# Optimization experiments

Measured on AMD Instinct MI355X. Metric: run time of the kernel, lower is better.

The kernel has to match this reference:

```python
import jax, jax.numpy as jnp
import numpy as np

UNIT_LEN = 16   # tokens per unit
DEPTH = 8       # units per path (path depth)
H = 256; NH = 8; DH = H // NH; FF = 1024; NL = 2; V = 32000; PAD = 0


def _pe(L, d):
    # standard sinusoidal positional encoding, seq-first [L,1,d]
    pos = jnp.arange(L, dtype=jnp.float32)[:, None]
    div = jnp.exp(jnp.arange(0, d, 2, dtype=jnp.float32) * (-np.log(10000.0) / d))
    pe = jnp.zeros((L, d), jnp.float32)
    pe = pe.at[:, 0::2].set(jnp.sin(pos * div)).at[:, 1::2].set(jnp.cos(pos * div))
    return pe[:, None, :]


def _ln(x, s, b):
    m = x.mean(-1, keepdims=True)
    v = jnp.mean((x - m) ** 2, -1, keepdims=True)
    return (x - m) * jax.lax.rsqrt(v + 1e-5) * s + b


def _layer(x, kpm, qkv_w, qkv_b, out_w, out_b, ln1_s, ln1_b, ff1_w, ff1_b, ff2_w, ff2_b, ln2_s, ln2_b):
    # x: [L,B,H] (seq-first, like torch TransformerEncoderLayer); kpm: [B,L] True = pad
    L, B, _ = x.shape
    qkv = x @ qkv_w.T + qkv_b
    q, k, v = jnp.split(qkv, 3, axis=-1)
    q = q.reshape(L, B, NH, DH); k = k.reshape(L, B, NH, DH); v = v.reshape(L, B, NH, DH)
    s = jnp.einsum('qbhd,kbhd->bhqk', q, k) / np.sqrt(DH)
    s = jnp.where(kpm[:, None, None, :], -1e9, s)
    a = jax.nn.softmax(s, axis=-1)
    o = jnp.einsum('bhqk,kbhd->qbhd', a, v).reshape(L, B, H) @ out_w.T + out_b
    x = _ln(x + o, ln1_s, ln1_b)
    f = jax.nn.relu(x @ ff1_w.T + ff1_b) @ ff2_w.T + ff2_b
    return _ln(x + f, ln2_s, ln2_b)


def _encoder(x, kpm, p):
    for i in range(p[0].shape[0]):
        x = _layer(x, kpm, *(w[i] for w in p))
    return x


def _mk_enc(key):
    ks = jax.random.split(key, 4)
    sc = 0.02
    return (jax.random.normal(ks[0], (NL, 3 * H, H)) * sc, jnp.zeros((NL, 3 * H)),
            jax.random.normal(ks[1], (NL, H, H)) * sc, jnp.zeros((NL, H)),
            jnp.ones((NL, H)), jnp.zeros((NL, H)),
            jax.random.normal(ks[2], (NL, FF, H)) * sc, jnp.zeros((NL, FF)),
            jax.random.normal(ks[3], (NL, H, FF)) * sc, jnp.zeros((NL, H)),
            jnp.ones((NL, H)), jnp.zeros((NL, H)))


NAMES = ['qkv_w', 'qkv_b', 'out_w', 'out_b', 'ln1_s', 'ln1_b', 'ff1_w', 'ff1_b', 'ff2_w', 'ff2_b', 'ln2_s', 'ln2_b']


def setup_inputs():
    key = jax.random.key(0)
    k = jax.random.split(key, 6)
    B = 8; UPD = 32; PPD = 64
    units = jax.random.randint(k[0], (UNIT_LEN, B * UPD), 0, V)
    paths = jax.random.randint(k[1], (DEPTH, B * PPD), 0, UPD)
    emb = jax.random.normal(k[2], (V, H)) * 0.02
    d = {'units': units, 'paths': paths, 'unit_per_data': UPD, 'path_per_data': PPD, 'emb': emb}
    for n_, a in zip(NAMES, _mk_enc(k[3])):
        d['ep_' + n_] = a
    for n_, a in zip(NAMES, _mk_enc(k[4])):
        d['od_' + n_] = a
    return d


def _forward(units, paths, unit_per_data, path_per_data, emb, ep, od):
    # _unit_to_path: expand each path into its units' token sequences (vectorized gather).
    P = paths.shape[1]
    col = (jnp.arange(P) // path_per_data) * unit_per_data + paths       # [DEPTH, P] global unit column
    ctx = units[:, col]                                                  # [UNIT_LEN, DEPTH, P]
    ctx = jnp.transpose(ctx, (1, 0, 2)).reshape(DEPTH * UNIT_LEN, P)     # concat units along the path
    mask = ctx == PAD                                                    # expaths key-padding mask
    x = emb[ctx] + _pe(ctx.shape[0], H)
    expaths = _encoder(x, mask.T, ep)
    # _cut_batch: concat each sample's unit token sequences into one order sequence.
    nb = units.shape[1] // unit_per_data
    order_tok = units.reshape(UNIT_LEN, nb, unit_per_data).transpose(2, 0, 1).reshape(unit_per_data * UNIT_LEN, nb)
    omask = order_tok == PAD
    y = emb[order_tok] + _pe(order_tok.shape[0], H)
    order_enc = _encoder(y, omask.T, od)
    return expaths, order_enc


def reference(units, paths, unit_per_data, path_per_data, emb,
              ep_qkv_w, ep_qkv_b, ep_out_w, ep_out_b, ep_ln1_s, ep_ln1_b, ep_ff1_w, ep_ff1_b, ep_ff2_w, ep_ff2_b, ep_ln2_s, ep_ln2_b,
              od_qkv_w, od_qkv_b, od_out_w, od_out_b, od_ln1_s, od_ln1_b, od_ff1_w, od_ff1_b, od_ff2_w, od_ff2_b, od_ln2_s, od_ln2_b):
    ep = (ep_qkv_w, ep_qkv_b, ep_out_w, ep_out_b, ep_ln1_s, ep_ln1_b, ep_ff1_w, ep_ff1_b, ep_ff2_w, ep_ff2_b, ep_ln2_s, ep_ln2_b)
    od = (od_qkv_w, od_qkv_b, od_out_w, od_out_b, od_ln1_s, od_ln1_b, od_ff1_w, od_ff1_b, od_ff2_w, od_ff2_b, od_ln2_s, od_ln2_b)
    return _forward(units, paths, unit_per_data, path_per_data, emb, ep, od)
```

## Files before the change

### kernel.cpp

```cpp
#include <hip/hip_runtime.h>
#include <math.h>

#define H      256
#define NH     8
#define DH     32
#define FFDIM  1024
#define L1     128
#define B1     512
#define L2     512
#define B2     8
#define N1     (L1*B1)
#define N2     (L2*B2)
#define RT1    (N1/128)
#define RT2    (N2/128)
#define QSCL   0.25506602273492887f

typedef unsigned short u16;
typedef unsigned short ushort4_t __attribute__((ext_vector_type(4)));
typedef unsigned short ushort8_t __attribute__((ext_vector_type(8)));
typedef short          short8_t  __attribute__((ext_vector_type(8)));
typedef float          f32x4     __attribute__((ext_vector_type(4)));

__device__ __forceinline__ float bf2f(u16 u) {
    union { unsigned int i; float f; } v; v.i = ((unsigned int)u) << 16; return v.f;
}
__device__ __forceinline__ u16 f2bf(float f) {
    union { float f; unsigned int i; } v; v.f = f;
    unsigned int x = v.i;
    return (u16)((x + 0x7fffu + ((x >> 16) & 1u)) >> 16);
}
__device__ __forceinline__ unsigned cvt_pk_bf16(float lo, float hi) {
    unsigned r;
    asm("v_cvt_pk_bf16_f32 %0, %1, %2" : "=v"(r) : "v"(lo), "v"(hi));
    return r;
}

__global__ __launch_bounds__(256) void k_f2bf8(
    const float* __restrict__ s0, const float* __restrict__ s1,
    const float* __restrict__ s2, const float* __restrict__ s3,
    const float* __restrict__ s4, const float* __restrict__ s5,
    const float* __restrict__ s6, const float* __restrict__ s7,
    u16* __restrict__ out)
{
    const int cums[9] = {0, 393216, 524288, 1048576, 1572864,
                         1966080, 2097152, 2621440, 3145728};
    const float* srcs[8] = {s0, s1, s2, s3, s4, s5, s6, s7};
    const int gbase = blockIdx.x * 1024;
    int seg = 0;
    #pragma unroll
    for (int i = 1; i < 8; ++i) if (gbase >= cums[i]) seg = i;
    const int idx = gbase + threadIdx.x * 4;
    const int off = idx - cums[seg];
    const float fs = ((seg == 0 || seg == 4) && (off % 196608) < 65536)
                   ? QSCL : 1.0f;
    const float4 v = *(const float4*)(srcs[seg] + off);
    ushort4_t o;
    o.x = f2bf(v.x * fs); o.y = f2bf(v.y * fs);
    o.z = f2bf(v.z * fs); o.w = f2bf(v.w * fs);
    *(ushort4_t*)(out + idx) = o;
}

__global__ __launch_bounds__(256) void k_scaleb(
    const float* __restrict__ b1, const float* __restrict__ b2,
    float* __restrict__ out)
{
    const int i = blockIdx.x * 256 + threadIdx.x;
    const float* src = (i < 1536) ? b1 : b2;
    const int j = (i < 1536) ? i : i - 1536;
    float v = src[j];
    if ((j % 768) < 256) v *= QSCL;
    out[i] = v;
}

__global__ __launch_bounds__(256) void k_gather(
    const int* __restrict__ units, const int* __restrict__ paths,
    const float* __restrict__ emb,
    u16* __restrict__ x1, u16* __restrict__ x2,
    int* __restrict__ tokb1, int* __restrict__ tokb2)
{
    const int wave = threadIdx.x >> 6, lane = threadIdx.x & 63;
    const int t = blockIdx.x * 4 + wave;
    int tokid, l;
    u16* xp; int* tokp;
    if (t < N1) {
        l = t / B1; const int b = t - l * B1;
        const int d = l >> 4, u = l & 15;
        const int col = (b >> 6) * 32 + paths[d * 512 + b];
        tokid = units[u * 256 + col];
        xp = x1 + (size_t)t * H; tokp = tokb1 + t;
    } else {
        const int t2 = t - N1;
        l = t2 / B2; const int b = t2 - l * B2;
        const int w = l >> 4, u = l & 15;
        tokid = units[u * 256 + b * 32 + w];
        xp = x2 + (size_t)t2 * H; tokp = tokb2 + t2;
    }
    if (lane == 0) *tokp = tokid;
    const int c = lane * 4;
    const float4 e = *(const float4*)(emb + (size_t)tokid * H + c);
    const float i0 = (float)(c >> 1);
    const float a0 = (float)l * expf(-0.07195578415606394f * i0);
    const float a1 = (float)l * expf(-0.07195578415606394f * (i0 + 1.0f));
    ushort4_t o;
    o.x = f2bf(e.x + sinf(a0));
    o.y = f2bf(e.y + cosf(a0));
    o.z = f2bf(e.z + sinf(a1));
    o.w = f2bf(e.w + cosf(a1));
    *(ushort4_t*)(xp + c) = o;
}

#define BUF_U16 8192
__global__ __launch_bounds__(256) void k_gemm_mfma(
    const u16* __restrict__ X1, const u16* __restrict__ X2,
    const u16* __restrict__ W1, const u16* __restrict__ W2,
    const float* __restrict__ b1, const float* __restrict__ b2,
    u16* __restrict__ Y1, u16* __restrict__ Y2,
    int K, int M, int relu)
{
    __shared__ __align__(16) u16 smem[17408];
    const int t = threadIdx.x;
    const int mtiles = M >> 7;
    const int nwg = gridDim.x;
    const int bid = blockIdx.x;
    const int wg = (bid & 7) * (nwg >> 3) + (bid >> 3);
    const int rt = wg / mtiles;
    const int bn = (wg % mtiles) * 128;
    const u16* X; const u16* W; const float* bias; u16* Y; int bm;
    if (rt < RT1) { X = X1; W = W1; bias = b1; Y = Y1; bm = rt * 128; }
    else          { X = X2; W = W2; bias = b2; Y = Y2; bm = (rt - RT1) * 128; }
    const int wave = t >> 6, lane = t & 63;
    const int wr = (wave >> 1) * 64, wc = (wave & 1) * 64;
    const int lrow = lane & 15;
    const int lg   = lane >> 4;

    const u16* gx[2]; const u16* gw[2];
    int ldsxo[2], ldswo[2];
    #pragma unroll
    for (int i = 0; i < 2; ++i) {
        const int c = wave * 2 + i;
        const int r = c * 16 + (lane >> 2);
        const int s = (lane & 3) ^ ((r >> 1) & 3);
        gx[i] = X + (size_t)(bm + r) * K + s * 8;
        gw[i] = W + (size_t)(bn + r) * K + s * 8;
        ldsxo[i] = c * 512;
        ldswo[i] = 4096 + c * 512;
    }
    int aoff[4], boff[4];
    #pragma unroll
    for (int m = 0; m < 4; ++m) {
        const int R = wr + m * 16 + lrow;
        aoff[m] = R * 32 + ((lg ^ ((R >> 1) & 3)) * 8);
    }
    #pragma unroll
    for (int n = 0; n < 4; ++n) {
        const int R = wc + n * 16 + lrow;
        boff[n] = 4096 + R * 32 + ((lg ^ ((R >> 1) & 3)) * 8);
    }

    f32x4 acc[4][4] = {};
    const int nt = K >> 5;

    #pragma unroll
    for (int i = 0; i < 2; ++i) {
        __builtin_amdgcn_global_load_lds(gx[i], &smem[ldsxo[i]], 16, 0, 0);
        __builtin_amdgcn_global_load_lds(gw[i], &smem[ldswo[i]], 16, 0, 0);
        gx[i] += 32; gw[i] += 32;
    }
    __syncthreads();

    int cur = 0;
    for (int ts = 0; ts < nt; ++ts) {
        if (ts + 1 < nt) {
            const int nb = (cur ^ 1) * BUF_U16;
            #pragma unroll
            for (int i = 0; i < 2; ++i) {
                __builtin_amdgcn_global_load_lds(gx[i], &smem[nb + ldsxo[i]], 16, 0, 0);
                __builtin_amdgcn_global_load_lds(gw[i], &smem[nb + ldswo[i]], 16, 0, 0);
                gx[i] += 32; gw[i] += 32;
            }
        }
        const int cb = cur * BUF_U16;
        short8_t a[4], b[4];
        #pragma unroll
        for (int m = 0; m < 4; ++m) a[m] = *(const short8_t*)&smem[cb + aoff[m]];
        #pragma unroll
        for (int n = 0; n < 4; ++n) b[n] = *(const short8_t*)&smem[cb + boff[n]];
        #pragma unroll
        for (int m = 0; m < 4; ++m)
            #pragma unroll
            for (int n = 0; n < 4; ++n)
                acc[m][n] = __builtin_amdgcn_mfma_f32_16x16x32_bf16(
                    a[m], b[n], acc[m][n], 0, 0, 0);
        __syncthreads();
        cur ^= 1;
    }

    float bv[4];
    #pragma unroll
    for (int n = 0; n < 4; ++n) bv[n] = bias[bn + wc + n * 16 + lrow];
    const int r0 = (lane >> 4) * 4;

    #pragma unroll
    for (int n = 0; n < 4; ++n) {
        const int lc = wc + n * 16 + lrow;
        #pragma unroll
        for (int m = 0; m < 4; ++m) {
            const int lr = wr + m * 16 + r0;
            #pragma unroll
            for (int j = 0; j < 4; ++j) {
                float v = acc[m][n][j] + bv[n];
                if (relu) v = fmaxf(v, 0.f);
                smem[(lr + j) * 136 + lc] = f2bf(v);
            }
        }
    }
    __syncthreads();
    #pragma unroll
    for (int it = 0; it < 8; ++it) {
        const int slot = it * 256 + t;
        const int row = slot >> 4;
        const int seg = (slot & 15) * 8;
        *(ushort8_t*)(Y + (size_t)(bm + row) * M + bn + seg) =
            *(const ushort8_t*)&smem[row * 136 + seg];
    }
}

__global__ __launch_bounds__(256) void k_attn_mfma(
    const u16* __restrict__ qkv1, const u16* __restrict__ qkv2,
    const int* __restrict__ tok1, const int* __restrict__ tok2,
    u16* __restrict__ out1, u16* __restrict__ out2)
{
    __shared__ __align__(16) u16 Ks[128][40];
    __shared__ __align__(16) u16 Vt[32][136];
    __shared__ __align__(16) u16 Pl[128][40];
    __shared__ int msk[128];
    const int t = threadIdx.x;
    const int wave = t >> 6, lane = t & 63;
    const int lq = lane & 15, lg = lane >> 4;
    const int bid = blockIdx.x;
    const u16* qkv; const int* tok; u16* out;
    int L, Bv, b, h, qt;
    if (bid < B1 * NH) {
        qkv = qkv1; tok = tok1; out = out1; L = L1; Bv = B1;
        qt = 0; b = bid >> 3; h = bid & 7;
    } else {
        const int r = bid - B1 * NH;
        qkv = qkv2; tok = tok2; out = out2; L = L2; Bv = B2;
        qt = r >> 6; const int bh = r & 63; b = bh >> 3; h = bh & 7;
    }
    const int q0 = qt * 128 + wave * 32;

    short8_t qf[2];
    #pragma unroll
    for (int n = 0; n < 2; ++n)
        qf[n] = *(const short8_t*)(qkv +
            (size_t)((q0 + n * 16 + lq) * Bv + b) * 768 + h * DH + lg * 8);

    f32x4 o[2][2] = {};
    float mrun[2] = {-1e9f, -1e9f};
    float lrun[2] = {0.f, 0.f};

    for (int kt = 0; kt < L; kt += 128) {
        #pragma unroll
        for (int it = 0; it < 2; ++it) {
            const int slot = t + it * 256;
            const int row = slot >> 2;
            const int seg = (slot & 3) * 8;
            const u16* base = qkv + (size_t)((kt + row) * Bv + b) * 768 + 256 + h * DH + seg;
            *(ushort8_t*)&Ks[row][seg] = *(const ushort8_t*)base;
            const ushort8_t v8 = *(const ushort8_t*)(base + 256);
            #pragma unroll
            for (int e = 0; e < 8; ++e) Vt[seg + e][row] = v8[e];
        }
        if (t < 128) msk[t] = tok[(size_t)(kt + t) * Bv + b];
        __syncthreads();

        uint2 preg[2][8];
        #pragma unroll
        for (int n = 0; n < 2; ++n) {
            f32x4 s[8];
            #pragma unroll
            for (int mp = 0; mp < 8; ++mp) {
                const short8_t kf = *(const short8_t*)&Ks[mp * 16 + lq][lg * 8];
                s[mp] = __builtin_amdgcn_mfma_f32_16x16x32_bf16(
                    kf, qf[n], (f32x4){0.f, 0.f, 0.f, 0.f}, 0, 0, 0);
            }
            float mx = -3.0e38f;
            #pragma unroll
            for (int mp = 0; mp < 8; ++mp) {
                #pragma unroll
                for (int j = 0; j < 4; ++j) {
                    float v = s[mp][j];
                    v = (msk[mp * 16 + lg * 4 + j] == 0) ? -1e9f : v;
                    s[mp][j] = v;
                    mx = fmaxf(mx, v);
                }
            }
            mx = fmaxf(mx, __shfl_xor(mx, 16));
            mx = fmaxf(mx, __shfl_xor(mx, 32));
            const float mnew = fmaxf(mrun[n], mx);
            const float fac = exp2f(mrun[n] - mnew);
            mrun[n] = mnew;
            lrun[n] *= fac;
            #pragma unroll
            for (int dt = 0; dt < 2; ++dt)
                #pragma unroll
                for (int j = 0; j < 4; ++j) o[dt][n][j] *= fac;
            float lsum = 0.f;
            #pragma unroll
            for (int mp = 0; mp < 8; ++mp) {
                const float p0 = exp2f(s[mp][0] - mnew);
                const float p1 = exp2f(s[mp][1] - mnew);
                const float p2 = exp2f(s[mp][2] - mnew);
                const float p3 = exp2f(s[mp][3] - mnew);
                lsum += (p0 + p1) + (p2 + p3);
                preg[n][mp].x = cvt_pk_bf16(p0, p1);
                preg[n][mp].y = cvt_pk_bf16(p2, p3);
            }
            lsum += __shfl_xor(lsum, 16);
            lsum += __shfl_xor(lsum, 32);
            lrun[n] += lsum;
        }

        #pragma unroll
        for (int kk = 0; kk < 4; ++kk) {
            #pragma unroll
            for (int n = 0; n < 2; ++n) {
                u16* prow = &Pl[wave * 32 + n * 16 + lq][0];
                *(uint2*)(prow + lg * 4)      = preg[n][2 * kk];
                *(uint2*)(prow + 16 + lg * 4) = preg[n][2 * kk + 1];
            }
            short8_t pf[2];
            #pragma unroll
            for (int n = 0; n < 2; ++n)
                pf[n] = *(const short8_t*)&Pl[wave * 32 + n * 16 + lq][lg * 8];
            #pragma unroll
            for (int dt = 0; dt < 2; ++dt) {
                const short8_t vf = *(const short8_t*)&Vt[dt * 16 + lq][kk * 32 + lg * 8];
                #pragma unroll
                for (int n = 0; n < 2; ++n)
                    o[dt][n] = __builtin_amdgcn_mfma_f32_16x16x32_bf16(
                        vf, pf[n], o[dt][n], 0, 0, 0);
            }
        }
        __syncthreads();
    }

    #pragma unroll
    for (int n = 0; n < 2; ++n) {
        const float inv = 1.f / lrun[n];
        const int q = q0 + n * 16 + lq;
        u16* op = out + (size_t)(q * Bv + b) * H + h * DH;
        #pragma unroll
        for (int dt = 0; dt < 2; ++dt)
            #pragma unroll
            for (int jj = 0; jj < 2; ++jj) {
                const unsigned pk = cvt_pk_bf16(o[dt][n][jj*2] * inv,
                                                o[dt][n][jj*2+1] * inv);
                *(unsigned*)(op + dt * 16 + lg * 4 + jj * 2) = pk;
            }
    }
}

__global__ __launch_bounds__(256) void k_add_ln(
    const u16* __restrict__ x1, const u16* __restrict__ x2,
    const u16* __restrict__ r1, const u16* __restrict__ r2,
    const float* __restrict__ gs1, const float* __restrict__ gs2,
    const float* __restrict__ gb1, const float* __restrict__ gb2,
    u16* __restrict__ y1, u16* __restrict__ y2)
{
    const int wave = threadIdx.x >> 6, lane = threadIdx.x & 63;
    size_t row = (size_t)blockIdx.x * 4 + wave;
    const u16 *x, *r; const float *gs, *gb; u16* y;
    if (row < N1) { x = x1; r = r1; gs = gs1; gb = gb1; y = y1; }
    else { row -= N1; x = x2; r = r2; gs = gs2; gb = gb2; y = y2; }
    const int c = lane * 4;
    const ushort4_t xv = *(const ushort4_t*)(x + row * H + c);
    const ushort4_t rv = *(const ushort4_t*)(r + row * H + c);
    float v[4] = { bf2f(xv.x) + bf2f(rv.x), bf2f(xv.y) + bf2f(rv.y),
                   bf2f(xv.z) + bf2f(rv.z), bf2f(xv.w) + bf2f(rv.w) };
    float sum = v[0] + v[1] + v[2] + v[3];
    float sq  = v[0]*v[0] + v[1]*v[1] + v[2]*v[2] + v[3]*v[3];
    #pragma unroll
    for (int off = 1; off < 64; off <<= 1) {
        sum += __shfl_xor(sum, off);
        sq  += __shfl_xor(sq, off);
    }
    const float mean = sum * (1.f / H);
    const float var  = sq * (1.f / H) - mean * mean;
    const float is   = rsqrtf(var + 1e-5f);
    const float4 sv = *(const float4*)(gs + c);
    const float4 bv = *(const float4*)(gb + c);
    ushort4_t o;
    o.x = f2bf((v[0] - mean) * is * sv.x + bv.x);
    o.y = f2bf((v[1] - mean) * is * sv.y + bv.y);
    o.z = f2bf((v[2] - mean) * is * sv.z + bv.z);
    o.w = f2bf((v[3] - mean) * is * sv.w + bv.w);
    *(ushort4_t*)(y + row * H + c) = o;
}

__global__ __launch_bounds__(256) void k_add_ln_f32(
    const u16* __restrict__ x1, const u16* __restrict__ x2,
    const u16* __restrict__ r1, const u16* __restrict__ r2,
    const float* __restrict__ gs1, const float* __restrict__ gs2,
    const float* __restrict__ gb1, const float* __restrict__ gb2,
    float* __restrict__ y)
{
    const int wave = threadIdx.x >> 6, lane = threadIdx.x & 63;
    const size_t grow = (size_t)blockIdx.x * 4 + wave;
    const int c = lane * 4;
    float* yp = y + grow * H + c;
    size_t row = grow;
    const u16 *x, *r; const float *gs, *gb;
    if (row < N1) { x = x1; r = r1; gs = gs1; gb = gb1; }
    else { row -= N1; x = x2; r = r2; gs = gs2; gb = gb2; }
    const ushort4_t xv = *(const ushort4_t*)(x + row * H + c);
    const ushort4_t rv = *(const ushort4_t*)(r + row * H + c);
    float v[4] = { bf2f(xv.x) + bf2f(rv.x), bf2f(xv.y) + bf2f(rv.y),
                   bf2f(xv.z) + bf2f(rv.z), bf2f(xv.w) + bf2f(rv.w) };
    float sum = v[0] + v[1] + v[2] + v[3];
    float sq  = v[0]*v[0] + v[1]*v[1] + v[2]*v[2] + v[3]*v[3];
    #pragma unroll
    for (int off = 1; off < 64; off <<= 1) {
        sum += __shfl_xor(sum, off);
        sq  += __shfl_xor(sq, off);
    }
    const float mean = sum * (1.f / H);
    const float var  = sq * (1.f / H) - mean * mean;
    const float is   = rsqrtf(var + 1e-5f);
    const float4 sv = *(const float4*)(gs + c);
    const float4 bv = *(const float4*)(gb + c);
    float4 o;
    o.x = (v[0] - mean) * is * sv.x + bv.x;
    o.y = (v[1] - mean) * is * sv.y + bv.y;
    o.z = (v[2] - mean) * is * sv.z + bv.z;
    o.w = (v[3] - mean) * is * sv.w + bv.w;
    *(float4*)yp = o;
}

extern "C" void kernel_launch(void* const* d_in, const int* in_sizes, int n_in,
                              void* d_out, int out_size, void* d_ws, size_t ws_size,
                              hipStream_t stream)
{
    const int* units = (const int*)d_in[0];
    const int* paths = (const int*)d_in[1];
    const float* emb = (const float*)d_in[4];
    const float* const* ep = (const float* const*)(d_in + 5);
    const float* const* od = (const float* const*)(d_in + 17);
    float* out = (float*)d_out;

    u16* bufX1   = (u16*)d_ws;
    u16* bufX2   = bufX1 + (size_t)N1 * H;
    u16* bufBig1 = bufX2 + (size_t)N2 * H;
    u16* bufBig2 = bufBig1 + (size_t)N1 * FFDIM;
    u16* bufO1   = bufBig2 + (size_t)N2 * FFDIM;
    u16* bufO2   = bufO1 + (size_t)N1 * H;
    int* tokb1   = (int*)(bufO2 + (size_t)N2 * H);
    int* tokb2   = tokb1 + N1;
    u16* wbuf    = (u16*)(tokb2 + N2);
    const int wqkv = 2 * 768 * H, wout = 2 * H * H,
              wff1 = 2 * FFDIM * H, wff2 = 2 * H * FFDIM;
    const int encstride = wqkv + wout + wff1 + wff2;
    float* qbias = (float*)(wbuf + 2 * (size_t)encstride);

    k_f2bf8<<<(2 * encstride) / 1024, 256, 0, stream>>>(
        ep[0], ep[2], ep[6], ep[8], od[0], od[2], od[6], od[8], wbuf);
    k_scaleb<<<12, 256, 0, stream>>>(ep[1], od[1], qbias);

    k_gather<<<(N1 + N2) / 4, 256, 0, stream>>>(units, paths, emb,
                                                bufX1, bufX2, tokb1, tokb2);

    for (int layer = 0; layer < 2; ++layer) {
        const u16* wb1 = wbuf;
        const u16* wb2 = wbuf + (size_t)encstride;
        const u16* qkvw1 = wb1 + (size_t)layer * 768 * H;
        const u16* qkvw2 = wb2 + (size_t)layer * 768 * H;
        const u16* outw1 = wb1 + wqkv + (size_t)layer * H * H;
        const u16* outw2 = wb2 + wqkv + (size_t)layer * H * H;
        const u16* ff1w1 = wb1 + wqkv + wout + (size_t)layer * FFDIM * H;
        const u16* ff1w2 = wb2 + wqkv + wout + (size_t)layer * FFDIM * H;
        const u16* ff2w1 = wb1 + wqkv + wout + wff1 + (size_t)layer * H * FFDIM;
        const u16* ff2w2 = wb2 + wqkv + wout + wff1 + (size_t)layer * H * FFDIM;
        const float* qkvb1 = qbias + (size_t)layer * 768;
        const float* qkvb2 = qbias + 1536 + (size_t)layer * 768;
        const float* outb1 = ep[3] + (size_t)layer * H;
        const float* outb2 = od[3] + (size_t)layer * H;
        const float* ln1s1 = ep[4] + (size_t)layer * H;
        const float* ln1s2 = od[4] + (size_t)layer * H;
        const float* ln1b1 = ep[5] + (size_t)layer * H;
        const float* ln1b2 = od[5] + (size_t)layer * H;
        const float* ff1b1 = ep[7] + (size_t)layer * FFDIM;
        const float* ff1b2 = od[7] + (size_t)layer * FFDIM;
        const float* ff2b1 = ep[9] + (size_t)layer * H;
        const float* ff2b2 = od[9] + (size_t)layer * H;
        const float* ln2s1 = ep[10] + (size_t)layer * H;
        const float* ln2s2 = od[10] + (size_t)layer * H;
        const float* ln2b1 = ep[11] + (size_t)layer * H;
        const float* ln2b2 = od[11] + (size_t)layer * H;

        k_gemm_mfma<<<(RT1 + RT2) * (768 / 128), 256, 0, stream>>>(
            bufX1, bufX2, qkvw1, qkvw2, qkvb1, qkvb2, bufBig1, bufBig2, H, 768, 0);
        k_attn_mfma<<<B1 * NH + B2 * NH * (L2 / 128), 256, 0, stream>>>(
            bufBig1, bufBig2, tokb1, tokb2, bufO1, bufO2);
        k_gemm_mfma<<<(RT1 + RT2) * (H / 128), 256, 0, stream>>>(
            bufO1, bufO2, outw1, outw2, outb1, outb2, bufBig1, bufBig2, H, H, 0);
        k_add_ln<<<(N1 + N2) / 4, 256, 0, stream>>>(
            bufX1, bufX2, bufBig1, bufBig2, ln1s1, ln1s2, ln1b1, ln1b2, bufX1, bufX2);
        k_gemm_mfma<<<(RT1 + RT2) * (FFDIM / 128), 256, 0, stream>>>(
            bufX1, bufX2, ff1w1, ff1w2, ff1b1, ff1b2, bufBig1, bufBig2, H, FFDIM, 1);
        k_gemm_mfma<<<(RT1 + RT2) * (H / 128), 256, 0, stream>>>(
            bufBig1, bufBig2, ff2w1, ff2w2, ff2b1, ff2b2, bufO1, bufO2, FFDIM, H, 0);
        if (layer == 1)
            k_add_ln_f32<<<(N1 + N2) / 4, 256, 0, stream>>>(
                bufX1, bufX2, bufO1, bufO2, ln2s1, ln2s2, ln2b1, ln2b2, out);
        else
            k_add_ln<<<(N1 + N2) / 4, 256, 0, stream>>>(
                bufX1, bufX2, bufO1, bufO2, ln2s1, ln2s2, ln2b1, ln2b2, bufX1, bufX2);
    }
}
```

Measured before the change: 565.6 us.

## Fuse output-projection and FF2 GEMMs with residual add and LayerNorm

Adds a GEMM kernel with 64x256 output tiles that covers the full hidden width, so each block can add the bias and residual, compute row mean and variance across two waves through shared memory, and write the LayerNorm result directly. It replaces the separate GEMM plus add-LN kernels, removing one intermediate write and read of the activation tensor and one launch per LN. The fused kernel uses larger tiles, so fewer blocks and more registers, and it reads the residual from the same buffer it overwrites. That in-place write is safe only because each block reads its own rows before writing them.

```diff
diff --git a/kernel.cpp b/kernel.cpp
--- a/kernel.cpp
+++ b/kernel.cpp
@@ -225,6 +225,213 @@
     }
 }
 
+#define BUF2_U16 10240
+template<int FP32OUT>
+__global__ __launch_bounds__(256) void k_gemm_ln(
+    const u16* __restrict__ X1, const u16* __restrict__ X2,
+    const u16* __restrict__ W1, const u16* __restrict__ W2,
+    const float* __restrict__ b1, const float* __restrict__ b2,
+    const u16* __restrict__ R1, const u16* __restrict__ R2,
+    const float* __restrict__ gs1, const float* __restrict__ gs2,
+    const float* __restrict__ gb1, const float* __restrict__ gb2,
+    u16* __restrict__ Y1, u16* __restrict__ Y2, float* __restrict__ Yf,
+    int K)
+{
+    __shared__ __align__(16) u16 smem[2 * BUF2_U16];
+    const int t = threadIdx.x;
+    const int nwg = gridDim.x;
+    const int bid = blockIdx.x;
+    const int wg = (bid & 7) * (nwg >> 3) + (bid >> 3);
+    const u16* X; const u16* W; const float* bias; const u16* res;
+    const float* gs; const float* gb; u16* Y; int bm; size_t growbase;
+    if (wg < N1 / 64) {
+        X = X1; W = W1; bias = b1; res = R1; gs = gs1; gb = gb1; Y = Y1;
+        bm = wg * 64; growbase = (size_t)bm;
+    } else {
+        X = X2; W = W2; bias = b2; res = R2; gs = gs2; gb = gb2; Y = Y2;
+        bm = (wg - N1 / 64) * 64; growbase = (size_t)N1 + bm;
+    }
+    const int wave = t >> 6, lane = t & 63;
+    const int wrow = (wave >> 1) * 32;
+    const int wcol = (wave & 1) * 128;
+    const int lrow = lane & 15;
+    const int lg   = lane >> 4;
+
+    const u16* gsrc[5]; int ldso[5];
+    #pragma unroll
+    for (int i = 0; i < 5; ++i) {
+        const int c = wave * 5 + i;
+        const int rr = lane >> 2;
+        const int s  = lane & 3;
+        if (c < 4) {
+            const int r = c * 16 + rr;
+            gsrc[i] = X + (size_t)(bm + r) * K + ((s ^ ((r >> 1) & 3)) * 8);
+        } else {
+            const int r = (c - 4) * 16 + rr;
+            gsrc[i] = W + (size_t)r * K + ((s ^ ((r >> 1) & 3)) * 8);
+        }
+        ldso[i] = c * 512;
+    }
+    int aoff[2], boff[8];
+    #pragma unroll
+    for (int m = 0; m < 2; ++m) {
+        const int R = wrow + m * 16 + lrow;
+        aoff[m] = R * 32 + ((lg ^ ((R >> 1) & 3)) * 8);
+    }
+    #pragma unroll
+    for (int n = 0; n < 8; ++n) {
+        const int R = wcol + n * 16 + lrow;
+        boff[n] = 2048 + R * 32 + ((lg ^ ((R >> 1) & 3)) * 8);
+    }
+
+    f32x4 acc[2][8] = {};
+    const int nt = K >> 5;
+
+    #pragma unroll
+    for (int i = 0; i < 5; ++i) {
+        __builtin_amdgcn_global_load_lds(gsrc[i], &smem[ldso[i]], 16, 0, 0);
+        gsrc[i] += 32;
+    }
+    __syncthreads();
+
+    int cur = 0;
+    for (int ts = 0; ts < nt; ++ts) {
+        if (ts + 1 < nt) {
+            const int nb = (cur ^ 1) * BUF2_U16;
+            #pragma unroll
+            for (int i = 0; i < 5; ++i) {
+                __builtin_amdgcn_global_load_lds(gsrc[i], &smem[nb + ldso[i]], 16, 0, 0);
+                gsrc[i] += 32;
+            }
+        }
+        const int cb = cur * BUF2_U16;
+        short8_t a[2], b[8];
+        #pragma unroll
+        for (int m = 0; m < 2; ++m) a[m] = *(const short8_t*)&smem[cb + aoff[m]];
+        #pragma unroll
+        for (int n = 0; n < 8; ++n) b[n] = *(const short8_t*)&smem[cb + boff[n]];
+        #pragma unroll
+        for (int m = 0; m < 2; ++m)
+            #pragma unroll
+            for (int n = 0; n < 8; ++n)
+                acc[m][n] = __builtin_amdgcn_mfma_f32_16x16x32_bf16(
+                    a[m], b[n], acc[m][n], 0, 0, 0);
+        __syncthreads();
+        cur ^= 1;
+    }
+
+    float bv[8], gsv[8], gbv[8];
+    #pragma unroll
+    for (int n = 0; n < 8; ++n) {
+        const int col = wcol + n * 16 + lrow;
+        bv[n] = bias[col]; gsv[n] = gs[col]; gbv[n] = gb[col];
+    }
+
+    #pragma unroll
+    for (int it = 0; it < 8; ++it) {
+        const int slot = it * 256 + t;
+        const int row = slot >> 5;
+        const int seg = (slot & 31) * 8;
+        *(ushort8_t*)&smem[row * 264 + seg] =
+            *(const ushort8_t*)(res + (size_t)(bm + row) * 256 + seg);
+    }
+    __syncthreads();
+
+    float* sums = (float*)&smem[16896];
+
+    const int r0 = lg * 4;
+    #pragma unroll
+    for (int m = 0; m < 2; ++m) {
+        #pragma unroll
+        for (int j = 0; j < 4; ++j) {
+            const int rowl = wrow + m * 16 + r0 + j;
+            float s = 0.f, q = 0.f;
+            #pragma unroll
+            for (int n = 0; n < 8; ++n) {
+                const int col = wcol + n * 16 + lrow;
+                float v = acc[m][n][j] + bv[n] + bf2f(smem[rowl * 264 + col]);
+                acc[m][n][j] = v;
+                s += v; q += v * v;
+            }
+            #pragma unroll
+            for (int off = 1; off < 16; off <<= 1) {
+                s += __shfl_xor(s, off);
+                q += __shfl_xor(q, off);
+            }
+            if (lrow == 0) {
+                sums[rowl * 4 + (wave & 1) * 2 + 0] = s;
+                sums[rowl * 4 + (wave & 1) * 2 + 1] = q;
+            }
+        }
+    }
+    __syncthreads();
+
+    if (FP32OUT == 0) {
+        #pragma unroll
+        for (int m = 0; m < 2; ++m) {
+            #pragma unroll
+            for (int j = 0; j < 4; ++j) {
+                const int rowl = wrow + m * 16 + r0 + j;
+                const float s = sums[rowl * 4 + 0] + sums[rowl * 4 + 2];
+                const float q = sums[rowl * 4 + 1] + sums[rowl * 4 + 3];
+                const float mean = s * (1.f / 256.f);
+                const float var  = q * (1.f / 256.f) - mean * mean;
+                const float is   = rsqrtf(var + 1e-5f);
+                #pragma unroll
+                for (int n = 0; n < 8; ++n) {
+                    const int col = wcol + n * 16 + lrow;
+                    const float y = (acc[m][n][j] - mean) * is * gsv[n] + gbv[n];
+                    smem[rowl * 264 + col] = f2bf(y);
+                }
+            }
+        }
+        __syncthreads();
+        #pragma unroll
+        for (int it = 0; it < 8; ++it) {
+            const int slot = it * 256 + t;
+            const int row = slot >> 5;
+            const int seg = (slot & 31) * 8;
+            *(ushort8_t*)(Y + (size_t)(bm + row) * 256 + seg) =
+                *(const ushort8_t*)&smem[row * 264 + seg];
+        }
+    } else {
+        float* fstage = (float*)smem;
+        #pragma unroll
+        for (int h = 0; h < 2; ++h) {
+            if ((wave & 1) == h) {
+                #pragma unroll
+                for (int m = 0; m < 2; ++m) {
+                    #pragma unroll
+                    for (int j = 0; j < 4; ++j) {
+                        const int rowl = wrow + m * 16 + r0 + j;
+                        const float s = sums[rowl * 4 + 0] + sums[rowl * 4 + 2];
+                        const float q = sums[rowl * 4 + 1] + sums[rowl * 4 + 3];
+                        const float mean = s * (1.f / 256.f);
+                        const float var  = q * (1.f / 256.f) - mean * mean;
+                        const float is   = rsqrtf(var + 1e-5f);
+                        #pragma unroll
+                        for (int n = 0; n < 8; ++n) {
+                            const int col = n * 16 + lrow;
+                            const float y = (acc[m][n][j] - mean) * is * gsv[n] + gbv[n];
+                            fstage[rowl * 130 + col] = y;
+                        }
+                    }
+                }
+            }
+            __syncthreads();
+            #pragma unroll
+            for (int it = 0; it < 8; ++it) {
+                const int slot = it * 256 + t;
+                const int row = slot >> 5;
+                const int seg = (slot & 31) * 4;
+                *(float4*)(Yf + (growbase + row) * 256 + h * 128 + seg) =
+                    *(const float4*)&fstage[row * 130 + seg];
+            }
+            __syncthreads();
+        }
+    }
+}
+
 __global__ __launch_bounds__(256) void k_attn_mfma(
     const u16* __restrict__ qkv1, const u16* __restrict__ qkv2,
     const int* __restrict__ tok1, const int* __restrict__ tok2,
@@ -360,82 +567,6 @@
                 *(unsigned*)(op + dt * 16 + lg * 4 + jj * 2) = pk;
             }
     }
-}
-
-__global__ __launch_bounds__(256) void k_add_ln(
-    const u16* __restrict__ x1, const u16* __restrict__ x2,
-    const u16* __restrict__ r1, const u16* __restrict__ r2,
-    const float* __restrict__ gs1, const float* __restrict__ gs2,
-    const float* __restrict__ gb1, const float* __restrict__ gb2,
-    u16* __restrict__ y1, u16* __restrict__ y2)
-{
-    const int wave = threadIdx.x >> 6, lane = threadIdx.x & 63;
-    size_t row = (size_t)blockIdx.x * 4 + wave;
-    const u16 *x, *r; const float *gs, *gb; u16* y;
-    if (row < N1) { x = x1; r = r1; gs = gs1; gb = gb1; y = y1; }
-    else { row -= N1; x = x2; r = r2; gs = gs2; gb = gb2; y = y2; }
-    const int c = lane * 4;
-    const ushort4_t xv = *(const ushort4_t*)(x + row * H + c);
-    const ushort4_t rv = *(const ushort4_t*)(r + row * H + c);
-    float v[4] = { bf2f(xv.x) + bf2f(rv.x), bf2f(xv.y) + bf2f(rv.y),
-                   bf2f(xv.z) + bf2f(rv.z), bf2f(xv.w) + bf2f(rv.w) };
-    float sum = v[0] + v[1] + v[2] + v[3];
-    float sq  = v[0]*v[0] + v[1]*v[1] + v[2]*v[2] + v[3]*v[3];
-    #pragma unroll
-    for (int off = 1; off < 64; off <<= 1) {
-        sum += __shfl_xor(sum, off);
-        sq  += __shfl_xor(sq, off);
-    }
-    const float mean = sum * (1.f / H);
-    const float var  = sq * (1.f / H) - mean * mean;
-    const float is   = rsqrtf(var + 1e-5f);
-    const float4 sv = *(const float4*)(gs + c);
-    const float4 bv = *(const float4*)(gb + c);
-    ushort4_t o;
-    o.x = f2bf((v[0] - mean) * is * sv.x + bv.x);
-    o.y = f2bf((v[1] - mean) * is * sv.y + bv.y);
-    o.z = f2bf((v[2] - mean) * is * sv.z + bv.z);
-    o.w = f2bf((v[3] - mean) * is * sv.w + bv.w);
-    *(ushort4_t*)(y + row * H + c) = o;
-}
-
-__global__ __launch_bounds__(256) void k_add_ln_f32(
-    const u16* __restrict__ x1, const u16* __restrict__ x2,
-    const u16* __restrict__ r1, const u16* __restrict__ r2,
-    const float* __restrict__ gs1, const float* __restrict__ gs2,
-    const float* __restrict__ gb1, const float* __restrict__ gb2,
-    float* __restrict__ y)
-{
-    const int wave = threadIdx.x >> 6, lane = threadIdx.x & 63;
-    const size_t grow = (size_t)blockIdx.x * 4 + wave;
-    const int c = lane * 4;
-    float* yp = y + grow * H + c;
-    size_t row = grow;
-    const u16 *x, *r; const float *gs, *gb;
-    if (row < N1) { x = x1; r = r1; gs = gs1; gb = gb1; }
-    else { row -= N1; x = x2; r = r2; gs = gs2; gb = gb2; }
-    const ushort4_t xv = *(const ushort4_t*)(x + row * H + c);
-    const ushort4_t rv = *(const ushort4_t*)(r + row * H + c);
-    float v[4] = { bf2f(xv.x) + bf2f(rv.x), bf2f(xv.y) + bf2f(rv.y),
-                   bf2f(xv.z) + bf2f(rv.z), bf2f(xv.w) + bf2f(rv.w) };
-    float sum = v[0] + v[1] + v[2] + v[3];
-    float sq  = v[0]*v[0] + v[1]*v[1] + v[2]*v[2] + v[3]*v[3];
-    #pragma unroll
-    for (int off = 1; off < 64; off <<= 1) {
-        sum += __shfl_xor(sum, off);
-        sq  += __shfl_xor(sq, off);
-    }
-    const float mean = sum * (1.f / H);
-    const float var  = sq * (1.f / H) - mean * mean;
-    const float is   = rsqrtf(var + 1e-5f);
-    const float4 sv = *(const float4*)(gs + c);
-    const float4 bv = *(const float4*)(gb + c);
-    float4 o;
-    o.x = (v[0] - mean) * is * sv.x + bv.x;
-    o.y = (v[1] - mean) * is * sv.y + bv.y;
-    o.z = (v[2] - mean) * is * sv.z + bv.z;
-    o.w = (v[3] - mean) * is * sv.w + bv.w;
-    *(float4*)yp = o;
 }
 
 extern "C" void kernel_launch(void* const* d_in, const int* in_sizes, int n_in,
@@ -502,19 +633,18 @@
             bufX1, bufX2, qkvw1, qkvw2, qkvb1, qkvb2, bufBig1, bufBig2, H, 768, 0);
         k_attn_mfma<<<B1 * NH + B2 * NH * (L2 / 128), 256, 0, stream>>>(
             bufBig1, bufBig2, tokb1, tokb2, bufO1, bufO2);
-        k_gemm_mfma<<<(RT1 + RT2) * (H / 128), 256, 0, stream>>>(
-            bufO1, bufO2, outw1, outw2, outb1, outb2, bufBig1, bufBig2, H, H, 0);
-        k_add_ln<<<(N1 + N2) / 4, 256, 0, stream>>>(
-            bufX1, bufX2, bufBig1, bufBig2, ln1s1, ln1s2, ln1b1, ln1b2, bufX1, bufX2);
+        k_gemm_ln<0><<<(N1 + N2) / 64, 256, 0, stream>>>(
+            bufO1, bufO2, outw1, outw2, outb1, outb2, bufX1, bufX2,
+            ln1s1, ln1s2, ln1b1, ln1b2, bufX1, bufX2, nullptr, H);
         k_gemm_mfma<<<(RT1 + RT2) * (FFDIM / 128), 256, 0, stream>>>(
             bufX1, bufX2, ff1w1, ff1w2, ff1b1, ff1b2, bufBig1, bufBig2, H, FFDIM, 1);
-        k_gemm_mfma<<<(RT1 + RT2) * (H / 128), 256, 0, stream>>>(
-            bufBig1, bufBig2, ff2w1, ff2w2, ff2b1, ff2b2, bufO1, bufO2, FFDIM, H, 0);
         if (layer == 1)
-            k_add_ln_f32<<<(N1 + N2) / 4, 256, 0, stream>>>(
-                bufX1, bufX2, bufO1, bufO2, ln2s1, ln2s2, ln2b1, ln2b2, out);
+            k_gemm_ln<1><<<(N1 + N2) / 64, 256, 0, stream>>>(
+                bufBig1, bufBig2, ff2w1, ff2w2, ff2b1, ff2b2, bufX1, bufX2,
+                ln2s1, ln2s2, ln2b1, ln2b2, nullptr, nullptr, out, FFDIM);
         else
-            k_add_ln<<<(N1 + N2) / 4, 256, 0, stream>>>(
-                bufX1, bufX2, bufO1, bufO2, ln2s1, ln2s2, ln2b1, ln2b2, bufX1, bufX2);
-    }
-}
+            k_gemm_ln<0><<<(N1 + N2) / 64, 256, 0, stream>>>(
+                bufBig1, bufBig2, ff2w1, ff2w2, ff2b1, ff2b2, bufX1, bufX2,
+                ln2s1, ln2s2, ln2b1, ln2b2, bufX1, bufX2, nullptr, FFDIM);
+    }
+}
```

New measurement: 592.6 us. 1.05x slower.

## Fuse FFN up and down projections into one kernel keeping hidden tile in LDS

Applied to the files above, without the earlier changes.

Replaces the two FFN GEMM launches with one kernel per 128-row tile. It computes each 128-wide chunk of the ReLU hidden activation, stages it in shared memory, and accumulates the down projection in registers. This avoids writing and re-reading the 1024-wide intermediate through global memory. In exchange the grid shrinks to one block per row tile (544 blocks), shared memory use rises to about 66KB, and the 128 fp32 accumulators per lane increase register pressure, so occupancy drops.

```diff
diff --git a/kernel.cpp b/kernel.cpp
--- a/kernel.cpp
+++ b/kernel.cpp
@@ -222,6 +222,196 @@
         const int seg = (slot & 15) * 8;
         *(ushort8_t*)(Y + (size_t)(bm + row) * M + bn + seg) =
             *(const ushort8_t*)&smem[row * 136 + seg];
+    }
+}
+
+__global__ __launch_bounds__(256) void k_ffn(
+    const u16* __restrict__ X1, const u16* __restrict__ X2,
+    const u16* __restrict__ W1a, const u16* __restrict__ W1b,
+    const float* __restrict__ b1a, const float* __restrict__ b1b,
+    const u16* __restrict__ W2a, const u16* __restrict__ W2b,
+    const float* __restrict__ b2a, const float* __restrict__ b2b,
+    u16* __restrict__ Y1, u16* __restrict__ Y2)
+{
+    __shared__ __align__(16) u16 smem[33792];
+    const int t = threadIdx.x;
+    const int nwg = gridDim.x;
+    const int bid = blockIdx.x;
+    const int wg = (bid & 7) * (nwg >> 3) + (bid >> 3);
+    const u16* X; const u16* W1; const float* bias1;
+    const u16* W2; const float* bias2; u16* Y; int bm;
+    if (wg < RT1) { X = X1; W1 = W1a; bias1 = b1a; W2 = W2a; bias2 = b2a;
+                    Y = Y1; bm = wg * 128; }
+    else          { X = X2; W1 = W1b; bias1 = b1b; W2 = W2b; bias2 = b2b;
+                    Y = Y2; bm = (wg - RT1) * 128; }
+    const int wave = t >> 6, lane = t & 63;
+    const int wr  = (wave >> 1) * 64;
+    const int wc  = (wave & 1) * 64;
+    const int wc2 = (wave & 1) * 128;
+    const int lrow = lane & 15;
+    const int lg   = lane >> 4;
+    const int r0   = lg * 4;
+
+    const int src1r[2] = { (wave*2+0)*16 + (lane >> 2), (wave*2+1)*16 + (lane >> 2) };
+    const int src1s[2] = { ((lane & 3) ^ ((src1r[0] >> 1) & 3)) * 8,
+                           ((lane & 3) ^ ((src1r[1] >> 1) & 3)) * 8 };
+    int ldsxo[2], ldswo[2];
+    #pragma unroll
+    for (int i = 0; i < 2; ++i) {
+        ldsxo[i] = (wave * 2 + i) * 512;
+        ldswo[i] = 4096 + (wave * 2 + i) * 512;
+    }
+    int aoff1[4], boff1[4];
+    #pragma unroll
+    for (int m = 0; m < 4; ++m) {
+        const int R = wr + m * 16 + lrow;
+        aoff1[m] = R * 32 + ((lg ^ ((R >> 1) & 3)) * 8);
+    }
+    #pragma unroll
+    for (int n = 0; n < 4; ++n) {
+        const int R = wc + n * 16 + lrow;
+        boff1[n] = 4096 + R * 32 + ((lg ^ ((R >> 1) & 3)) * 8);
+    }
+    int src2r[4], src2s[4], lds2o[4];
+    #pragma unroll
+    for (int i = 0; i < 4; ++i) {
+        const int c2 = wave * 4 + i;
+        src2r[i] = c2 * 16 + (lane >> 2);
+        src2s[i] = ((lane & 3) ^ ((src2r[i] >> 1) & 3)) * 8;
+        lds2o[i] = c2 * 512;
+    }
+    int aoff2[4], boff2[8];
+    #pragma unroll
+    for (int m = 0; m < 4; ++m)
+        aoff2[m] = 16384 + (wr + m * 16 + lrow) * 136;
+    #pragma unroll
+    for (int n = 0; n < 8; ++n) {
+        const int R = wc2 + n * 16 + lrow;
+        boff2[n] = R * 32 + ((lg ^ ((R >> 1) & 3)) * 8);
+    }
+    float bv2[8];
+    #pragma unroll
+    for (int n = 0; n < 8; ++n) bv2[n] = bias2[wc2 + n * 16 + lrow];
+
+    f32x4 acc2[4][8] = {};
+
+    for (int ch = 0; ch < 8; ++ch) {
+        const u16* gx[2]; const u16* gw[2];
+        #pragma unroll
+        for (int i = 0; i < 2; ++i) {
+            gx[i] = X + (size_t)(bm + src1r[i]) * 256 + src1s[i];
+            gw[i] = W1 + (size_t)(ch * 128 + src1r[i]) * 256 + src1s[i];
+        }
+        f32x4 acc1[4][4] = {};
+        #pragma unroll
+        for (int i = 0; i < 2; ++i) {
+            __builtin_amdgcn_global_load_lds(gx[i], &smem[ldsxo[i]], 16, 0, 0);
+            __builtin_amdgcn_global_load_lds(gw[i], &smem[ldswo[i]], 16, 0, 0);
+            gx[i] += 32; gw[i] += 32;
+        }
+        __syncthreads();
+        int cur = 0;
+        #pragma unroll
+        for (int ts = 0; ts < 8; ++ts) {
+            if (ts + 1 < 8) {
+                const int nb = (cur ^ 1) * BUF_U16;
+                #pragma unroll
+                for (int i = 0; i < 2; ++i) {
+                    __builtin_amdgcn_global_load_lds(gx[i], &smem[nb + ldsxo[i]], 16, 0, 0);
+                    __builtin_amdgcn_global_load_lds(gw[i], &smem[nb + ldswo[i]], 16, 0, 0);
+                    gx[i] += 32; gw[i] += 32;
+                }
+            }
+            const int cb = cur * BUF_U16;
+            short8_t a[4], b[4];
+            #pragma unroll
+            for (int m = 0; m < 4; ++m) a[m] = *(const short8_t*)&smem[cb + aoff1[m]];
+            #pragma unroll
+            for (int n = 0; n < 4; ++n) b[n] = *(const short8_t*)&smem[cb + boff1[n]];
+            #pragma unroll
+            for (int m = 0; m < 4; ++m)
+                #pragma unroll
+                for (int n = 0; n < 4; ++n)
+                    acc1[m][n] = __builtin_amdgcn_mfma_f32_16x16x32_bf16(
+                        a[m], b[n], acc1[m][n], 0, 0, 0);
+            __syncthreads();
+            cur ^= 1;
+        }
+
+        const u16* gw2[4];
+        #pragma unroll
+        for (int i = 0; i < 4; ++i)
+            gw2[i] = W2 + (size_t)src2r[i] * 1024 + ch * 128 + src2s[i];
+        #pragma unroll
+        for (int i = 0; i < 4; ++i) {
+            __builtin_amdgcn_global_load_lds(gw2[i], &smem[lds2o[i]], 16, 0, 0);
+            gw2[i] += 32;
+        }
+        #pragma unroll
+        for (int n = 0; n < 4; ++n) {
+            const float bv1 = bias1[ch * 128 + wc + n * 16 + lrow];
+            const int lc = wc + n * 16 + lrow;
+            #pragma unroll
+            for (int m = 0; m < 4; ++m) {
+                const int lr = wr + m * 16 + r0;
+                #pragma unroll
+                for (int j = 0; j < 4; ++j) {
+                    const float v = fmaxf(acc1[m][n][j] + bv1, 0.f);
+                    smem[16384 + (lr + j) * 136 + lc] = f2bf(v);
+                }
+            }
+        }
+        __syncthreads();
+
+        cur = 0;
+        #pragma unroll
+        for (int ks = 0; ks < 4; ++ks) {
+            if (ks + 1 < 4) {
+                const int nb = (cur ^ 1) * BUF_U16;
+                #pragma unroll
+                for (int i = 0; i < 4; ++i) {
+                    __builtin_amdgcn_global_load_lds(gw2[i], &smem[nb + lds2o[i]], 16, 0, 0);
+                    gw2[i] += 32;
+                }
+            }
+            const int cb = cur * BUF_U16;
+            short8_t a[4], b[8];
+            #pragma unroll
+            for (int m = 0; m < 4; ++m)
+                a[m] = *(const short8_t*)&smem[aoff2[m] + ks * 32 + lg * 8];
+            #pragma unroll
+            for (int n = 0; n < 8; ++n)
+                b[n] = *(const short8_t*)&smem[cb + boff2[n]];
+            #pragma unroll
+            for (int m = 0; m < 4; ++m)
+                #pragma unroll
+                for (int n = 0; n < 8; ++n)
+                    acc2[m][n] = __builtin_amdgcn_mfma_f32_16x16x32_bf16(
+                        a[m], b[n], acc2[m][n], 0, 0, 0);
+            __syncthreads();
+            cur ^= 1;
+        }
+    }
+
+    #pragma unroll
+    for (int n = 0; n < 8; ++n) {
+        const int lc = wc2 + n * 16 + lrow;
+        #pragma unroll
+        for (int m = 0; m < 4; ++m) {
+            const int lr = wr + m * 16 + r0;
+            #pragma unroll
+            for (int j = 0; j < 4; ++j)
+                smem[(lr + j) * 264 + lc] = f2bf(acc2[m][n][j] + bv2[n]);
+        }
+    }
+    __syncthreads();
+    #pragma unroll
+    for (int it = 0; it < 16; ++it) {
+        const int slot = it * 256 + t;
+        const int row = slot >> 5;
+        const int seg = (slot & 31) * 8;
+        *(ushort8_t*)(Y + (size_t)(bm + row) * 256 + seg) =
+            *(const ushort8_t*)&smem[row * 264 + seg];
     }
 }
 
@@ -506,10 +696,9 @@
             bufO1, bufO2, outw1, outw2, outb1, outb2, bufBig1, bufBig2, H, H, 0);
         k_add_ln<<<(N1 + N2) / 4, 256, 0, stream>>>(
             bufX1, bufX2, bufBig1, bufBig2, ln1s1, ln1s2, ln1b1, ln1b2, bufX1, bufX2);
-        k_gemm_mfma<<<(RT1 + RT2) * (FFDIM / 128), 256, 0, stream>>>(
-            bufX1, bufX2, ff1w1, ff1w2, ff1b1, ff1b2, bufBig1, bufBig2, H, FFDIM, 1);
-        k_gemm_mfma<<<(RT1 + RT2) * (H / 128), 256, 0, stream>>>(
-            bufBig1, bufBig2, ff2w1, ff2w2, ff2b1, ff2b2, bufO1, bufO2, FFDIM, H, 0);
+        k_ffn<<<RT1 + RT2, 256, 0, stream>>>(
+            bufX1, bufX2, ff1w1, ff1w2, ff1b1, ff1b2,
+            ff2w1, ff2w2, ff2b1, ff2b2, bufO1, bufO2);
         if (layer == 1)
             k_add_ln_f32<<<(N1 + N2) / 4, 256, 0, stream>>>(
                 bufX1, bufX2, bufO1, bufO2, ln2s1, ln2s2, ln2b1, ln2b2, out);
```

New measurement: 660.4 us. +16.8%, slower.
